# Performance work log

Hardware: AMD Instinct MI355X
Metric: run time of the kernel (lower is better)

Reference implementation:

```python
import jax, jax.numpy as jnp
import numpy as np
from jax import lax

B, HI, WI, D = 8, 64, 64, 128
HO, WO = HI // 2, WI // 2
N_IN, N_OUT = HI * WI, HO * WO
NUM_ITERS = 3
EPS = 1e-6


def _build_indices(Ho, Wo):
    # replicates _build_q_and_in_idx: per coarse position, 9 relative offsets
    dys = np.repeat(np.arange(-1, 2), 3)
    dxs = np.tile(np.arange(-1, 2), 3)
    oy = np.arange(Ho)[:, None, None]
    ox = np.arange(Wo)[None, :, None]
    ny = oy + dys
    nx = ox + dxs
    valid = (ny >= 0) & (ny < Ho) & (nx >= 0) & (nx < Wo)  # (Ho,Wo,9)
    coarse = np.where(valid, ny * Wo + nx, 0)
    base = (oy * Wo + ox) * 9
    g9 = np.where(valid, base + np.arange(9), 0).reshape(-1, 9)
    c9 = coarse.reshape(-1, 9)
    q_idx = np.stack([np.tile(g9, (1, 4))] * 4)
    col_idx = np.stack([np.tile(c9, (1, 4))] * 4)
    in_idx = np.stack([np.tile(np.where(valid, coarse * 4 + h, 0).reshape(-1, 9), (1, 4)) for h in range(4)])
    return q_idx.astype(np.int32), in_idx.astype(np.int32), col_idx.astype(np.int32)


Q_IDX, IN_IDX, COL_IDX = _build_indices(HO, WO)
# NATTEN kernel-3 neighborhoods: window center clamped to stay in-bounds.
NY = np.clip(np.arange(HO) - 1, 0, HO - 3)[:, None] + np.arange(3)  # (HO,3)
NX = np.clip(np.arange(WO) - 1, 0, WO - 3)[:, None] + np.arange(3)  # (WO,3)


def _ln(x, g, b, eps=1e-5):
    mu = x.mean(-1, keepdims=True)
    var = ((x - mu) ** 2).mean(-1, keepdims=True)
    return (x - mu) * lax.rsqrt(var + eps) * g + b


def _forward(x, seed_w, wq, wk, wv, w1, b1, w2, b2, ln_in_g, ln_in_b, ln_out_g, ln_out_b, rpb, tau):
    ny, nx = jnp.asarray(NY), jnp.asarray(NX)
    q_idx = jnp.asarray(Q_IDX)

    def unfold(t):  # (B,HI,WI,D) -> (B,4,HO,WO,D); head = ky*2+kx (F.unfold order)
        return t.reshape(B, HO, 2, WO, 2, D).transpose(0, 2, 4, 1, 3, 5).reshape(B, 4, HO, WO, D)

    k = unfold((_ln(x, ln_in_g, ln_in_b) @ wk.T).reshape(B, HI, WI, D))
    v = unfold((x @ wv.T).reshape(B, HI, WI, D))
    k_n = k[:, :, ny][:, :, :, :, nx]  # (B,4,HO,3,WO,3,D)
    v_n = v[:, :, ny][:, :, :, :, nx]

    x_map = x.reshape(B, HI, WI, D).transpose(0, 3, 1, 2)
    seed = lax.conv_general_dilated(x_map, seed_w, (2, 2), ((1, 1), (1, 1)),
                                    dimension_numbers=('NCHW', 'OIHW', 'NCHW'))
    x_out = _ln(seed.reshape(B, D, N_OUT).transpose(0, 2, 1), ln_out_g, ln_out_b)

    scale = jnp.exp(tau)
    attn36 = a_col_h = None
    for _ in range(NUM_ITERS):
        q = (_ln(x_out, ln_out_g, ln_out_b) @ wq.T).reshape(B, HO, WO, D)
        # na2d_qk (q broadcast over the 4 heads) + relative position bias
        logits = jnp.einsum('byxd,bhykxld->bhyxkl', q, k_n).reshape(B, 4, HO, WO, 9) + rpb.reshape(1, 4, 1, 1, 9)
        attn = jax.nn.softmax(logits * scale, axis=-1) + EPS
        flat = attn.reshape(B, 4, N_OUT * 9)
        attn36 = jnp.take_along_axis(
            flat, jnp.broadcast_to(q_idx.reshape(1, 4, -1), (B, 4, N_OUT * 36)), axis=-1
        ).reshape(B, 4, N_OUT, 36)
        a_col_h = attn36 / (attn36.sum(axis=(1, 3), keepdims=True) + EPS)
        attn9 = a_col_h[..., :9].reshape(B, 4, HO, WO, 3, 3)
        # na2d_av then sum over heads
        updates = jnp.einsum('bhyxkl,bhykxld->byxd', attn9, v_n).reshape(B, N_OUT, D)
        x_out = x_out + updates
        h1 = jax.nn.gelu(x_out @ w1.T + b1, approximate=False)
        x_out = x_out + _ln(h1 @ w2.T + b2, ln_out_g, ln_out_b)
    return x_out, attn36, a_col_h


def setup_inputs() -> dict:
    key = jax.random.key(0)
    ks = jax.random.split(key, 8)
    n = lambda k, shape, s: jax.random.normal(k, shape, jnp.float32) * s
    D2 = 2 * D
    return {
        'x': jax.random.normal(ks[0], (B, N_IN, D), jnp.float32),
        'seed_w': n(ks[1], (D, D, 3, 3), (2.0 / (9 * D)) ** 0.5),
        'wq': n(ks[2], (D, D), D ** -0.5),
        'wk': n(ks[3], (D, D), D ** -0.5),
        'wv': n(ks[4], (D, D), D ** -0.5),
        'w1': n(ks[5], (D2, D), D ** -0.5),
        'b1': jnp.zeros((D2,), jnp.float32),
        'w2': n(ks[6], (D, D2), D2 ** -0.5),
        'b2': jnp.zeros((D,), jnp.float32),
        'ln_in_g': jnp.ones((D,), jnp.float32),
        'ln_in_b': jnp.zeros((D,), jnp.float32),
        'ln_out_g': jnp.ones((D,), jnp.float32),
        'ln_out_b': jnp.zeros((D,), jnp.float32),
        'rpb': n(ks[7], (4, 9), 0.02),
        'tau': jnp.float32(np.log(D ** -0.5)),
    }


def reference(x, seed_w, wq, wk, wv, w1, b1, w2, b2, ln_in_g, ln_in_b, ln_out_g, ln_out_b, rpb, tau):
    x_out, attn36, a_col_h = _forward(x, seed_w, wq, wk, wv, w1, b1, w2, b2,
                                      ln_in_g, ln_in_b, ln_out_g, ln_out_b, rpb, tau)
    # A_col: scatter_add over dim 1 -> A_col[b, in_idx[i,j], j] += a_col_h[b,i,j]
    rows = jnp.asarray(IN_IDX).reshape(4 * N_OUT, 36)
    cols = jnp.broadcast_to(jnp.arange(36), rows.shape)
    A_col = jnp.zeros((B, N_IN, N_OUT), x.dtype).at[:, rows, cols].add(a_col_h.reshape(B, 4 * N_OUT, 36))
    # A_row: scatter_add over dim 2 -> A_row[b, i, col_idx[i,j]] += attn36[b,i,j]
    ri = jnp.broadcast_to(jnp.arange(4 * N_OUT)[:, None], (4 * N_OUT, 36))
    A_row = jnp.zeros((B, N_IN, N_OUT), x.dtype).at[:, ri, jnp.asarray(COL_IDX).reshape(4 * N_OUT, 36)].add(
        attn36.reshape(B, 4 * N_OUT, 36))
    return x_out, A_row, A_col
```

## Files before the change

### kernel.cpp

```cpp
#include <hip/hip_runtime.h>
#include <hip/hip_bf16.h>
#include <math.h>

#define BB   8
#define HI_  64
#define WI_  64
#define DD   128
#define HO_  32
#define WO_  32
#define NIN  4096
#define NOUT 1024
#define LN_EPS 1e-5f
#define ATT_EPS 1e-6f

typedef short bf16x8 __attribute__((ext_vector_type(8)));
typedef float f32x4  __attribute__((ext_vector_type(4)));

__device__ __forceinline__ ushort f2bf(float f) {
    union { float f; unsigned u; } a; a.f = f;
    unsigned u = a.u;
    return (ushort)((u + 0x7FFFu + ((u >> 16) & 1u)) >> 16);
}
__device__ __forceinline__ float bf2f(ushort u) {
    union { unsigned u; float f; } a; a.u = ((unsigned)u) << 16;
    return a.f;
}

__global__ __launch_bounds__(256)
void wconvert_kernel(const float* __restrict__ wq, const float* __restrict__ wk,
                     const float* __restrict__ wv, const float* __restrict__ w1,
                     const float* __restrict__ w2, const float* __restrict__ sw,
                     ushort* __restrict__ dst)
{
    int i = blockIdx.x * 256 + threadIdx.x;
    float v;
    if (i < 16384)        v = wk[i];
    else if (i < 32768)   v = wv[i - 16384];
    else if (i < 49152)   v = wq[i - 32768];
    else if (i < 81920)   v = w1[i - 49152];
    else if (i < 114688)  v = w2[i - 81920];
    else {
        int j = i - 114688;
        int n = j / 1152;
        int rem = j - n * 1152;
        int tap = rem >> 7, di = rem & 127;
        v = sw[((size_t)(n * DD + di)) * 9 + tap];
    }
    dst[i] = f2bf(v);
}

__global__ __launch_bounds__(256)
void prep_kernel(const float* __restrict__ x, const ushort* __restrict__ wkb,
                 const ushort* __restrict__ wvb, const ushort* __restrict__ wcb,
                 const float* __restrict__ ligg, const float* __restrict__ libb,
                 const float* __restrict__ logg, const float* __restrict__ lobb,
                 ushort* __restrict__ kbuf, ushort* __restrict__ vbuf,
                 float* __restrict__ xout)
{
    __shared__ __align__(16) char arena[62208];
    const int tid = threadIdx.x;
    const int wid = tid >> 6, lane = tid & 63;
    const int lr = lane & 15, lk = (lane >> 4) << 3;

    if (blockIdx.x < 512) {
        ushort (*Araw)[136] = (ushort (*)[136])(arena);
        ushort (*Aln)[136]  = (ushort (*)[136])(arena + 17408);
        float  (*rstat)[2]  = (float  (*)[2])(arena + 34816);
        const int row0 = blockIdx.x * 64;

        float4 xv[8];
        #pragma unroll
        for (int i = 0; i < 8; ++i) {
            int l = tid + i * 256;
            int r = l >> 5, c4 = (l & 31) << 2;
            float4 v = *(const float4*)(x + (size_t)(row0 + r) * DD + c4);
            xv[i] = v;
            ushort4 o; o.x = f2bf(v.x); o.y = f2bf(v.y); o.z = f2bf(v.z); o.w = f2bf(v.w);
            *(ushort4*)&Araw[r][c4] = o;
            float s  = v.x + v.y + v.z + v.w;
            float s2 = v.x * v.x + v.y * v.y + v.z * v.z + v.w * v.w;
            #pragma unroll
            for (int o2 = 16; o2 > 0; o2 >>= 1) {
                s  += __shfl_down(s,  o2, 32);
                s2 += __shfl_down(s2, o2, 32);
            }
            if ((tid & 31) == 0) {
                float mu = s * (1.f / DD);
                float var = s2 * (1.f / DD) - mu * mu;
                rstat[r][0] = mu; rstat[r][1] = rsqrtf(var + LN_EPS);
            }
        }
        __syncthreads();
        #pragma unroll
        for (int i = 0; i < 8; ++i) {
            int l = tid + i * 256;
            int r = l >> 5, c4 = (l & 31) << 2;
            float mu = rstat[r][0], rs = rstat[r][1];
            float4 v = xv[i];
            ushort4 o;
            o.x = f2bf((v.x - mu) * rs * ligg[c4 + 0] + libb[c4 + 0]);
            o.y = f2bf((v.y - mu) * rs * ligg[c4 + 1] + libb[c4 + 1]);
            o.z = f2bf((v.z - mu) * rs * ligg[c4 + 2] + libb[c4 + 2]);
            o.w = f2bf((v.w - mu) * rs * ligg[c4 + 3] + libb[c4 + 3]);
            *(ushort4*)&Aln[r][c4] = o;
        }
        __syncthreads();

        const int wm = (wid & 1) * 32, wn = (wid >> 1) * 64;
        f32x4 ak[2][4] = {}, av[2][4] = {};
        #pragma unroll
        for (int ks = 0; ks < 4; ++ks) {
            int kk = ks * 32 + lk;
            bf16x8 aL[2], aR[2];
            #pragma unroll
            for (int mi = 0; mi < 2; ++mi) {
                aL[mi] = *(const bf16x8*)&Aln[wm + mi * 16 + lr][kk];
                aR[mi] = *(const bf16x8*)&Araw[wm + mi * 16 + lr][kk];
            }
            #pragma unroll
            for (int ni = 0; ni < 4; ++ni) {
                bf16x8 bK = *(const bf16x8*)(wkb + (size_t)(wn + ni * 16 + lr) * DD + kk);
                bf16x8 bV = *(const bf16x8*)(wvb + (size_t)(wn + ni * 16 + lr) * DD + kk);
                #pragma unroll
                for (int mi = 0; mi < 2; ++mi) {
                    ak[mi][ni] = __builtin_amdgcn_mfma_f32_16x16x32_bf16(aL[mi], bK, ak[mi][ni], 0, 0, 0);
                    av[mi][ni] = __builtin_amdgcn_mfma_f32_16x16x32_bf16(aR[mi], bV, av[mi][ni], 0, 0, 0);
                }
            }
        }
        #pragma unroll
        for (int mi = 0; mi < 2; ++mi) {
            #pragma unroll
            for (int ni = 0; ni < 4; ++ni) {
                int n = wn + ni * 16 + (lane & 15);
                #pragma unroll
                for (int r = 0; r < 4; ++r) {
                    int m = row0 + wm + mi * 16 + ((lane >> 4) << 2) + r;
                    int b = m >> 12, pix = m & 4095;
                    int iy = pix >> 6, ix = pix & 63;
                    int h = ((iy & 1) << 1) | (ix & 1);
                    int cp = ((iy >> 1) << 5) | (ix >> 1);
                    size_t orow = ((size_t)(b * 4 + h) << 10) + cp;
                    kbuf[orow * DD + n] = f2bf(ak[mi][ni][r]);
                    vbuf[orow * DD + n] = f2bf(av[mi][ni][r]);
                }
            }
        }
    } else {
        ushort (*As)[72]   = (ushort (*)[72])(arena);
        ushort (*Bs)[72]   = (ushort (*)[72])(arena + 9216);
        float  (*es)[132]  = (float  (*)[132])(arena + 27648);
        float  (*rstat)[2] = (float  (*)[2])(arena + 61440);
        const int row0 = (blockIdx.x - 512) * 64;
        const int wm = (wid & 1) * 32, wn = (wid >> 1) * 64;
        f32x4 acc[2][4] = {};

        for (int k0 = 0; k0 < 1152; k0 += 64) {
            #pragma unroll
            for (int i = 0; i < 4; ++i) {
                int l = tid + i * 256;
                int r = l >> 4, c4 = (l & 15) << 2;
                int m = row0 + r;
                int b = m >> 10, p = m & 1023;
                int y = p >> 5, xx = p & 31;
                int kg = k0 + c4;
                int tap = kg >> 7, di = kg & 127;
                int ky = tap / 3, kx = tap - ky * 3;
                int iy = 2 * y + ky - 1, ix = 2 * xx + kx - 1;
                float4 v;
                if ((unsigned)iy < (unsigned)HI_ && (unsigned)ix < (unsigned)WI_)
                    v = *(const float4*)(x + ((size_t)b * NIN + iy * WI_ + ix) * DD + di);
                else v = make_float4(0.f, 0.f, 0.f, 0.f);
                ushort4 o; o.x = f2bf(v.x); o.y = f2bf(v.y); o.z = f2bf(v.z); o.w = f2bf(v.w);
                *(ushort4*)&As[r][c4] = o;
            }
            #pragma unroll
            for (int i = 0; i < 4; ++i) {
                int l = tid + i * 256;
                int r = l >> 3, c8 = (l & 7) << 3;
                *(uint4*)&Bs[r][c8] = *(const uint4*)(wcb + (size_t)r * 1152 + k0 + c8);
            }
            __syncthreads();
            #pragma unroll
            for (int ks = 0; ks < 2; ++ks) {
                int kk = ks * 32 + lk;
                bf16x8 aF[2];
                aF[0] = *(const bf16x8*)&As[wm + lr][kk];
                aF[1] = *(const bf16x8*)&As[wm + 16 + lr][kk];
                #pragma unroll
                for (int ni = 0; ni < 4; ++ni) {
                    bf16x8 bF = *(const bf16x8*)&Bs[wn + ni * 16 + lr][kk];
                    acc[0][ni] = __builtin_amdgcn_mfma_f32_16x16x32_bf16(aF[0], bF, acc[0][ni], 0, 0, 0);
                    acc[1][ni] = __builtin_amdgcn_mfma_f32_16x16x32_bf16(aF[1], bF, acc[1][ni], 0, 0, 0);
                }
            }
            __syncthreads();
        }
        #pragma unroll
        for (int mi = 0; mi < 2; ++mi)
            #pragma unroll
            for (int ni = 0; ni < 4; ++ni) {
                int n = wn + ni * 16 + (lane & 15);
                #pragma unroll
                for (int r = 0; r < 4; ++r)
                    es[wm + mi * 16 + ((lane >> 4) << 2) + r][n] = acc[mi][ni][r];
            }
        __syncthreads();
        {
            int r = tid >> 2, q = tid & 3;
            float s = 0.f, s2 = 0.f;
            #pragma unroll
            for (int c = 0; c < 32; ++c) { float v = es[r][q * 32 + c]; s += v; s2 += v * v; }
            s += __shfl_down(s, 1, 64); s2 += __shfl_down(s2, 1, 64);
            s += __shfl_down(s, 2, 64); s2 += __shfl_down(s2, 2, 64);
            if (q == 0) {
                float mu = s * (1.f / DD);
                float var = s2 * (1.f / DD) - mu * mu;
                rstat[r][0] = mu; rstat[r][1] = rsqrtf(var + LN_EPS);
            }
        }
        __syncthreads();
        #pragma unroll
        for (int i = 0; i < 8; ++i) {
            int l = tid + i * 256;
            int r = l >> 5, c4 = (l & 31) << 2;
            float mu = rstat[r][0], rs = rstat[r][1];
            float4 o;
            o.x = (es[r][c4 + 0] - mu) * rs * logg[c4 + 0] + lobb[c4 + 0];
            o.y = (es[r][c4 + 1] - mu) * rs * logg[c4 + 1] + lobb[c4 + 1];
            o.z = (es[r][c4 + 2] - mu) * rs * logg[c4 + 2] + lobb[c4 + 2];
            o.w = (es[r][c4 + 3] - mu) * rs * logg[c4 + 3] + lobb[c4 + 3];
            *(float4*)(xout + (size_t)(row0 + r) * DD + c4) = o;
        }
    }
}

template<int LAST>
__global__ __launch_bounds__(256)
void iter_kernel(float* __restrict__ xout, const ushort* __restrict__ kbuf,
                 const ushort* __restrict__ vbuf, const ushort* __restrict__ wqb,
                 const ushort* __restrict__ w1b, const ushort* __restrict__ w2b,
                 const float* __restrict__ b1, const float* __restrict__ b2,
                 const float* __restrict__ lg_, const float* __restrict__ lb_,
                 const float* __restrict__ rpb, const float* __restrict__ tau,
                 float* __restrict__ gbuf, float* __restrict__ denb,
                 float* __restrict__ out)
{
    const int bid = blockIdx.x;
    const int b = bid >> 6, cy = (bid >> 1) & 31, cx0 = (bid & 1) << 4;
    const int ry0 = min(max(cy - 1, 0), HO_ - 3);
    const int tid = threadIdx.x;
    const int wid = tid >> 6, lane = tid & 63;
    const int lr = lane & 15, lk = (lane >> 4) << 3;

    __shared__ float  xsf[17][132];
    __shared__ ushort Aq[32][136];
    __shared__ ushort qs[17][136];
    __shared__ float  rstat[17][2];
    __shared__ float  lgp[16][36];
    __shared__ float  lg0[36];
    __shared__ float  sm0[4];
    __shared__ ushort h1s[16][264];
    __shared__ float  es[16][132];

    for (int l = tid; l < 544; l += 256) {
        int r = l >> 5, c4 = (l & 31) << 2;
        int g = b * NOUT + (r < 16 ? cy * 32 + cx0 + r : 0);
        *(float4*)&xsf[r][c4] = *(const float4*)(xout + (size_t)g * DD + c4);
    }
    __syncthreads();
    if (tid < 68) {
        int r = tid >> 2, q = tid & 3;
        float s = 0.f, s2 = 0.f;
        #pragma unroll
        for (int c = 0; c < 32; ++c) { float v = xsf[r][q * 32 + c]; s += v; s2 += v * v; }
        s += __shfl_down(s, 1, 64); s2 += __shfl_down(s2, 1, 64);
        s += __shfl_down(s, 2, 64); s2 += __shfl_down(s2, 2, 64);
        if (q == 0) {
            float mu = s * (1.f / DD);
            float var = s2 * (1.f / DD) - mu * mu;
            rstat[r][0] = mu; rstat[r][1] = rsqrtf(var + LN_EPS);
        }
    }
    __syncthreads();
    for (int l = tid; l < 544; l += 256) {
        int r = l >> 5, c4 = (l & 31) << 2;
        float mu = rstat[r][0], rs = rstat[r][1];
        ushort4 o;
        o.x = f2bf((xsf[r][c4 + 0] - mu) * rs * lg_[c4 + 0] + lb_[c4 + 0]);
        o.y = f2bf((xsf[r][c4 + 1] - mu) * rs * lg_[c4 + 1] + lb_[c4 + 1]);
        o.z = f2bf((xsf[r][c4 + 2] - mu) * rs * lg_[c4 + 2] + lb_[c4 + 2]);
        o.w = f2bf((xsf[r][c4 + 3] - mu) * rs * lg_[c4 + 3] + lb_[c4 + 3]);
        *(ushort4*)&Aq[r][c4] = o;
    }
    __syncthreads();

    {
        const int wn = wid * 32;
        f32x4 acc[2][2] = {};
        #pragma unroll
        for (int ks = 0; ks < 4; ++ks) {
            int kk = ks * 32 + lk;
            bf16x8 aF0 = *(const bf16x8*)&Aq[lr][kk];
            bf16x8 aF1 = *(const bf16x8*)&Aq[16 + lr][kk];
            #pragma unroll
            for (int ni = 0; ni < 2; ++ni) {
                bf16x8 bF = *(const bf16x8*)(wqb + (size_t)(wn + ni * 16 + lr) * DD + kk);
                acc[0][ni] = __builtin_amdgcn_mfma_f32_16x16x32_bf16(aF0, bF, acc[0][ni], 0, 0, 0);
                acc[1][ni] = __builtin_amdgcn_mfma_f32_16x16x32_bf16(aF1, bF, acc[1][ni], 0, 0, 0);
            }
        }
        #pragma unroll
        for (int mi = 0; mi < 2; ++mi)
            #pragma unroll
            for (int ni = 0; ni < 2; ++ni) {
                int n = wn + ni * 16 + (lane & 15);
                #pragma unroll
                for (int r = 0; r < 4; ++r) {
                    int m = mi * 16 + ((lane >> 4) << 2) + r;
                    if (m < 17) qs[m][n] = f2bf(acc[mi][ni][r]);
                }
            }
    }
    __syncthreads();

    for (int task = tid; task < 612; task += 256) {
        const ushort *kp, *qp;
        int cl = 0, h, jj;
        if (task < 576) {
            cl = task / 36; int t2 = task - cl * 36;
            h = t2 / 9; jj = t2 - h * 9;
            int ky = jj / 3, kx = jj - ky * 3;
            int c = cx0 + cl;
            int nx = min(max(c - 1, 0), WO_ - 3) + kx;
            kp = kbuf + (((size_t)(b * 4 + h) << 10) + (ry0 + ky) * 32 + nx) * DD;
            qp = &qs[cl][0];
        } else {
            int t2 = task - 576;
            h = t2 / 9; jj = t2 - h * 9;
            int ky = jj / 3, kx = jj - ky * 3;
            kp = kbuf + (((size_t)(b * 4 + h) << 10) + ky * 32 + kx) * DD;
            qp = &qs[16][0];
        }
        float s = 0.f;
        #pragma unroll 4
        for (int d = 0; d < 128; d += 8) {
            uint4 ku = *(const uint4*)(kp + d);
            uint4 qu = *(const uint4*)(qp + d);
            const ushort* kk2 = (const ushort*)&ku;
            const ushort* qq2 = (const ushort*)&qu;
            #pragma unroll
            for (int t = 0; t < 8; ++t) s += bf2f(kk2[t]) * bf2f(qq2[t]);
        }
        if (task < 576) lgp[cl][h * 9 + jj] = s;
        else            lg0[task - 576] = s;
    }
    __syncthreads();

    if (tid < 68) {
        float scale = expf(tau[0]);
        int h; const float* lptr; int cl = 0;
        if (tid < 64) { cl = tid >> 2; h = tid & 3; lptr = &lgp[cl][h * 9]; }
        else          { h = tid - 64; lptr = &lg0[h * 9]; }
        float tmpv[9], mx = -1e30f;
        #pragma unroll
        for (int jj = 0; jj < 9; ++jj) {
            float v = (lptr[jj] + rpb[h * 9 + jj]) * scale;
            tmpv[jj] = v; mx = fmaxf(mx, v);
        }
        float ss = 0.f;
        #pragma unroll
        for (int jj = 0; jj < 9; ++jj) { tmpv[jj] = expf(tmpv[jj] - mx); ss += tmpv[jj]; }
        float inv = 1.f / ss;
        if (tid < 64) {
            #pragma unroll
            for (int jj = 0; jj < 9; ++jj) lgp[cl][h * 9 + jj] = tmpv[jj] * inv + ATT_EPS;
        } else sm0[h] = tmpv[0] * inv + ATT_EPS;
    }
    __syncthreads();

    if (tid < 64) {
        int cl = tid >> 2, h = tid & 3;
        int c = cx0 + cl;
        float s = 0.f, gv[9];
        #pragma unroll
        for (int jj = 0; jj < 9; ++jj) {
            int dy = jj / 3 - 1, dx = jj % 3 - 1;
            bool valid = ((unsigned)(cy + dy) < (unsigned)HO_) && ((unsigned)(c + dx) < (unsigned)WO_);
            float v = valid ? lgp[cl][h * 9 + jj] : sm0[h];
            gv[jj] = v; s += v;
        }
        float tot = s;
        tot += __shfl_xor(tot, 1, 4);
        tot += __shfl_xor(tot, 2, 4);
        float dd = 4.f * tot + ATT_EPS;
        if (h == 0) denb[b * NOUT + cy * 32 + cx0 + cl] = dd;
        float inv = 1.f / dd;
        float* gp = gbuf + (((size_t)(b * 4 + h) << 10) + cy * 32 + c) * 9;
        #pragma unroll
        for (int jj = 0; jj < 9; ++jj) {
            gp[jj] = gv[jj];
            lgp[cl][h * 9 + jj] = gv[jj] * inv;
        }
    }
    __syncthreads();

    {
        int cl = tid >> 4, d0 = (tid & 15) << 3;
        int c = cx0 + cl;
        int rx0 = min(max(c - 1, 0), WO_ - 3);
        float acc8[8] = {};
        #pragma unroll
        for (int h = 0; h < 4; ++h)
            #pragma unroll
            for (int jj = 0; jj < 9; ++jj) {
                float cf = lgp[cl][h * 9 + jj];
                int ky = jj / 3, kx = jj - ky * 3;
                const ushort* vp = vbuf + (((size_t)(b * 4 + h) << 10) + (ry0 + ky) * 32 + rx0 + kx) * DD + d0;
                uint4 v0 = *(const uint4*)(vp);
                const ushort* vs0 = (const ushort*)&v0;
                #pragma unroll
                for (int t = 0; t < 8; ++t) acc8[t] += cf * bf2f(vs0[t]);
            }
        #pragma unroll
        for (int t = 0; t < 8; t += 4) {
            float4 o = *(float4*)&xsf[cl][d0 + t];
            o.x += acc8[t]; o.y += acc8[t + 1]; o.z += acc8[t + 2]; o.w += acc8[t + 3];
            *(float4*)&xsf[cl][d0 + t] = o;
        }
    }
    __syncthreads();

    for (int l = tid; l < 512; l += 256) {
        int r = l >> 5, c4 = (l & 31) << 2;
        ushort4 o;
        o.x = f2bf(xsf[r][c4 + 0]); o.y = f2bf(xsf[r][c4 + 1]);
        o.z = f2bf(xsf[r][c4 + 2]); o.w = f2bf(xsf[r][c4 + 3]);
        *(ushort4*)&Aq[r][c4] = o;
    }
    __syncthreads();
    {
        const int wn = wid * 64;
        f32x4 acc[4] = {};
        #pragma unroll
        for (int ks = 0; ks < 4; ++ks) {
            int kk = ks * 32 + lk;
            bf16x8 a0 = *(const bf16x8*)&Aq[lr][kk];
            #pragma unroll
            for (int ni = 0; ni < 4; ++ni) {
                bf16x8 bF = *(const bf16x8*)(w1b + (size_t)(wn + ni * 16 + lr) * DD + kk);
                acc[ni] = __builtin_amdgcn_mfma_f32_16x16x32_bf16(a0, bF, acc[ni], 0, 0, 0);
            }
        }
        #pragma unroll
        for (int ni = 0; ni < 4; ++ni) {
            int n = wn + ni * 16 + (lane & 15);
            float bv = b1[n];
            #pragma unroll
            for (int r = 0; r < 4; ++r) {
                int m = ((lane >> 4) << 2) + r;
                float v = acc[ni][r] + bv;
                v = 0.5f * v * (1.f + erff(v * 0.70710678118654752f));
                h1s[m][n] = f2bf(v);
            }
        }
    }
    __syncthreads();

    {
        const int wn = wid * 32;
        f32x4 acc[2] = {};
        #pragma unroll
        for (int ks = 0; ks < 8; ++ks) {
            int kk = ks * 32 + lk;
            bf16x8 a0 = *(const bf16x8*)&h1s[lr][kk];
            #pragma unroll
            for (int ni = 0; ni < 2; ++ni) {
                bf16x8 bF = *(const bf16x8*)(w2b + (size_t)(wn + ni * 16 + lr) * 256 + kk);
                acc[ni] = __builtin_amdgcn_mfma_f32_16x16x32_bf16(a0, bF, acc[ni], 0, 0, 0);
            }
        }
        #pragma unroll
        for (int ni = 0; ni < 2; ++ni) {
            int n = wn + ni * 16 + (lane & 15);
            float bv = b2[n];
            #pragma unroll
            for (int r = 0; r < 4; ++r)
                es[((lane >> 4) << 2) + r][n] = acc[ni][r] + bv;
        }
    }
    __syncthreads();
    if (tid < 128) {
        int r = tid >> 3, qq = tid & 7;
        float s = 0.f, s2 = 0.f;
        #pragma unroll
        for (int c = 0; c < 16; ++c) { float v = es[r][qq * 16 + c]; s += v; s2 += v * v; }
        s += __shfl_down(s, 1, 64); s2 += __shfl_down(s2, 1, 64);
        s += __shfl_down(s, 2, 64); s2 += __shfl_down(s2, 2, 64);
        s += __shfl_down(s, 4, 64); s2 += __shfl_down(s2, 4, 64);
        if (qq == 0) {
            float mu = s * (1.f / DD);
            float var = s2 * (1.f / DD) - mu * mu;
            rstat[r][0] = mu; rstat[r][1] = rsqrtf(var + LN_EPS);
        }
    }
    __syncthreads();
    for (int l = tid; l < 512; l += 256) {
        int r = l >> 5, c4 = (l & 31) << 2;
        float mu = rstat[r][0], rs = rstat[r][1];
        size_t off = ((size_t)(b * NOUT + cy * 32 + cx0 + r)) * DD + c4;
        float4 o;
        o.x = xsf[r][c4 + 0] + (es[r][c4 + 0] - mu) * rs * lg_[c4 + 0] + lb_[c4 + 0];
        o.y = xsf[r][c4 + 1] + (es[r][c4 + 1] - mu) * rs * lg_[c4 + 1] + lb_[c4 + 1];
        o.z = xsf[r][c4 + 2] + (es[r][c4 + 2] - mu) * rs * lg_[c4 + 2] + lb_[c4 + 2];
        o.w = xsf[r][c4 + 3] + (es[r][c4 + 3] - mu) * rs * lg_[c4 + 3] + lb_[c4 + 3];
        *(float4*)(xout + off) = o;
        if (LAST) *(float4*)(out + off) = o;
    }
}

__global__ __launch_bounds__(256)
void arowcol_kernel(const float* __restrict__ gbuf, const float* __restrict__ denb,
                    float* __restrict__ Arow, float* __restrict__ Acol)
{
    const int tid = threadIdx.x;
    __shared__ int   cols[9];
    __shared__ float vals[9];
    __shared__ float wred[9][4];
    if (blockIdx.x < 32768) {
        const int bi = blockIdx.x;
        const int b = bi >> 12, i = bi & 4095;
        const int h = i >> 10, p = i & 1023;
        const int cy = p >> 5, cx = p & 31;
        if (tid < 9) {
            int dy = tid / 3 - 1, dx = tid % 3 - 1;
            bool valid = ((unsigned)(cy + dy) < (unsigned)HO_) && ((unsigned)(cx + dx) < (unsigned)WO_);
            cols[tid] = valid ? (cy + dy) * WO_ + (cx + dx) : 0;
            vals[tid] = 4.f * gbuf[(((size_t)(b * 4 + h) << 10) + p) * 9 + tid];
        }
        __syncthreads();
        float* row = Arow + (size_t)bi * NOUT;
        int c4 = tid << 2;
        float o[4] = {};
        #pragma unroll
        for (int e = 0; e < 4; ++e)
            #pragma unroll
            for (int jj = 0; jj < 9; ++jj)
                if (cols[jj] == c4 + e) o[e] += vals[jj];
        *(float4*)(row + c4) = make_float4(o[0], o[1], o[2], o[3]);
    } else {
        const int br = blockIdx.x - 32768;
        const int b = br >> 12, r = br & 4095;
        const int h = r & 3, coarse = r >> 2;
        const int cy = coarse >> 5, cx = coarse & 31;
        if (tid < 9) {
            int dy = tid / 3 - 1, dx = tid % 3 - 1;
            int py = cy - dy, px = cx - dx;
            float v = 0.f;
            if ((unsigned)py < (unsigned)HO_ && (unsigned)px < (unsigned)WO_) {
                int p = py * WO_ + px;
                v = gbuf[(((size_t)(b * 4 + h) << 10) + p) * 9 + tid] / denb[b * NOUT + p];
            }
            vals[tid] = v;
        }
        if (r == 0) {
            float part[9] = {};
            for (int p = tid; p < NOUT; p += 256) {
                float invd = 1.f / denb[b * NOUT + p];
                int py = p >> 5, px = p & 31;
                #pragma unroll
                for (int jj = 0; jj < 9; ++jj) {
                    int dy = jj / 3 - 1, dx = jj % 3 - 1;
                    bool valid = ((unsigned)(py + dy) < (unsigned)HO_) && ((unsigned)(px + dx) < (unsigned)WO_);
                    if (!valid) part[jj] += invd;
                }
            }
            #pragma unroll
            for (int jj = 0; jj < 9; ++jj) {
                float s = part[jj];
                #pragma unroll
                for (int o = 32; o > 0; o >>= 1) s += __shfl_down(s, o, 64);
                if ((tid & 63) == 0) wred[jj][tid >> 6] = s;
            }
            __syncthreads();
            if (tid < 9) {
                float s = wred[tid][0] + wred[tid][1] + wred[tid][2] + wred[tid][3];
                float H = 0.f;
                for (int h2 = 0; h2 < 4; ++h2)
                    H += gbuf[(((size_t)(b * 4 + h2)) << 10) * 9];
                vals[tid] += H * s;
            }
        }
        __syncthreads();
        float* row = Acol + (size_t)br * NOUT;
        int c4 = tid << 2;
        float o[4];
        #pragma unroll
        for (int e = 0; e < 4; ++e) {
            int c = c4 + e;
            o[e] = (c < 36) ? vals[c % 9] : 0.f;
        }
        *(float4*)(row + c4) = make_float4(o[0], o[1], o[2], o[3]);
    }
}

extern "C" void kernel_launch(void* const* d_in, const int* in_sizes, int n_in,
                              void* d_out, int out_size, void* d_ws, size_t ws_size,
                              hipStream_t stream)
{
    const float* x        = (const float*)d_in[0];
    const float* seed_w   = (const float*)d_in[1];
    const float* wq       = (const float*)d_in[2];
    const float* wk       = (const float*)d_in[3];
    const float* wv       = (const float*)d_in[4];
    const float* w1       = (const float*)d_in[5];
    const float* b1       = (const float*)d_in[6];
    const float* w2       = (const float*)d_in[7];
    const float* b2       = (const float*)d_in[8];
    const float* ln_in_g  = (const float*)d_in[9];
    const float* ln_in_b  = (const float*)d_in[10];
    const float* ln_out_g = (const float*)d_in[11];
    const float* ln_out_b = (const float*)d_in[12];
    const float* rpb      = (const float*)d_in[13];
    const float* tau      = (const float*)d_in[14];

    float* out  = (float*)d_out;
    float* Arow = out + (size_t)BB * NOUT * DD;
    float* Acol = Arow + (size_t)BB * NIN * NOUT;

    float* ws    = (float*)d_ws;
    float* xout  = ws;
    float* gbuf  = xout + (size_t)BB * NOUT * DD;
    float* denb  = gbuf + (size_t)BB * 4 * NOUT * 9;
    ushort* wb   = (ushort*)(denb + BB * NOUT);
    ushort* wkb  = wb;
    ushort* wvb  = wb + 16384;
    ushort* wqb  = wb + 32768;
    ushort* w1b  = wb + 49152;
    ushort* w2b  = wb + 81920;
    ushort* wcb  = wb + 114688;

    ushort* kbuf = (ushort*)Arow;
    ushort* vbuf = kbuf + (size_t)4194304;

    wconvert_kernel<<<1024, 256, 0, stream>>>(wq, wk, wv, w1, w2, seed_w, wb);
    prep_kernel<<<640, 256, 0, stream>>>(x, wkb, wvb, wcb, ln_in_g, ln_in_b,
                                         ln_out_g, ln_out_b, kbuf, vbuf, xout);

    for (int it = 0; it < 3; ++it) {
        if (it < 2)
            iter_kernel<0><<<BB * HO_ * 2, 256, 0, stream>>>(
                xout, kbuf, vbuf, wqb, w1b, w2b, b1, b2, ln_out_g, ln_out_b,
                rpb, tau, gbuf, denb, out);
        else
            iter_kernel<1><<<BB * HO_ * 2, 256, 0, stream>>>(
                xout, kbuf, vbuf, wqb, w1b, w2b, b1, b2, ln_out_g, ln_out_b,
                rpb, tau, gbuf, denb, out);
    }

    arowcol_kernel<<<2 * BB * NIN, 256, 0, stream>>>(gbuf, denb, Arow, Acol);
}
```

Measured before the change: 192.7 us.

## Fold query projection into keys once in prep instead of per iteration

Uses the identity (ln(x) Wq^T)·k = ln(x)·(Wq^T k), precomputing K2 = K·Wq once in the prep kernel with a transposed bf16 Wq. Each of the three iteration kernels then skips its per-block Q projection GEMM and uses the normalized slot features directly as the query. This trades three small GEMMs per iteration for one larger extra GEMM in prep, plus an extra bf16 rounding step on the keys that may shift numerics.

```diff
diff --git a/kernel.cpp b/kernel.cpp
--- a/kernel.cpp
+++ b/kernel.cpp
@@ -36,7 +36,8 @@
     float v;
     if (i < 16384)        v = wk[i];
     else if (i < 32768)   v = wv[i - 16384];
-    else if (i < 49152)   v = wq[i - 32768];
+    else if (i < 49152) { int j = i - 32768; int d = j >> 7, n = j & 127;
+                          v = wq[n * DD + d]; }
     else if (i < 81920)   v = w1[i - 49152];
     else if (i < 114688)  v = w2[i - 81920];
     else {
@@ -51,10 +52,11 @@
 
 __global__ __launch_bounds__(256)
 void prep_kernel(const float* __restrict__ x, const ushort* __restrict__ wkb,
-                 const ushort* __restrict__ wvb, const ushort* __restrict__ wcb,
+                 const ushort* __restrict__ wvb, const ushort* __restrict__ wqTb,
+                 const ushort* __restrict__ wcb,
                  const float* __restrict__ ligg, const float* __restrict__ libb,
                  const float* __restrict__ logg, const float* __restrict__ lobb,
-                 ushort* __restrict__ kbuf, ushort* __restrict__ vbuf,
+                 ushort* __restrict__ k2buf, ushort* __restrict__ vbuf,
                  float* __restrict__ xout)
 {
     __shared__ __align__(16) char arena[62208];
@@ -107,44 +109,90 @@
         __syncthreads();
 
         const int wm = (wid & 1) * 32, wn = (wid >> 1) * 64;
-        f32x4 ak[2][4] = {}, av[2][4] = {};
-        #pragma unroll
-        for (int ks = 0; ks < 4; ++ks) {
-            int kk = ks * 32 + lk;
-            bf16x8 aL[2], aR[2];
-            #pragma unroll
-            for (int mi = 0; mi < 2; ++mi) {
-                aL[mi] = *(const bf16x8*)&Aln[wm + mi * 16 + lr][kk];
-                aR[mi] = *(const bf16x8*)&Araw[wm + mi * 16 + lr][kk];
-            }
-            #pragma unroll
-            for (int ni = 0; ni < 4; ++ni) {
-                bf16x8 bK = *(const bf16x8*)(wkb + (size_t)(wn + ni * 16 + lr) * DD + kk);
-                bf16x8 bV = *(const bf16x8*)(wvb + (size_t)(wn + ni * 16 + lr) * DD + kk);
+        {
+            f32x4 ak[2][4] = {}, av[2][4] = {};
+            #pragma unroll
+            for (int ks = 0; ks < 4; ++ks) {
+                int kk = ks * 32 + lk;
+                bf16x8 aL[2], aR[2];
                 #pragma unroll
                 for (int mi = 0; mi < 2; ++mi) {
-                    ak[mi][ni] = __builtin_amdgcn_mfma_f32_16x16x32_bf16(aL[mi], bK, ak[mi][ni], 0, 0, 0);
-                    av[mi][ni] = __builtin_amdgcn_mfma_f32_16x16x32_bf16(aR[mi], bV, av[mi][ni], 0, 0, 0);
-                }
-            }
-        }
-        #pragma unroll
-        for (int mi = 0; mi < 2; ++mi) {
-            #pragma unroll
-            for (int ni = 0; ni < 4; ++ni) {
-                int n = wn + ni * 16 + (lane & 15);
-                #pragma unroll
-                for (int r = 0; r < 4; ++r) {
-                    int m = row0 + wm + mi * 16 + ((lane >> 4) << 2) + r;
-                    int b = m >> 12, pix = m & 4095;
-                    int iy = pix >> 6, ix = pix & 63;
-                    int h = ((iy & 1) << 1) | (ix & 1);
-                    int cp = ((iy >> 1) << 5) | (ix >> 1);
-                    size_t orow = ((size_t)(b * 4 + h) << 10) + cp;
-                    kbuf[orow * DD + n] = f2bf(ak[mi][ni][r]);
-                    vbuf[orow * DD + n] = f2bf(av[mi][ni][r]);
-                }
-            }
+                    aL[mi] = *(const bf16x8*)&Aln[wm + mi * 16 + lr][kk];
+                    aR[mi] = *(const bf16x8*)&Araw[wm + mi * 16 + lr][kk];
+                }
+                #pragma unroll
+                for (int ni = 0; ni < 4; ++ni) {
+                    bf16x8 bK = *(const bf16x8*)(wkb + (size_t)(wn + ni * 16 + lr) * DD + kk);
+                    bf16x8 bV = *(const bf16x8*)(wvb + (size_t)(wn + ni * 16 + lr) * DD + kk);
+                    #pragma unroll
+                    for (int mi = 0; mi < 2; ++mi) {
+                        ak[mi][ni] = __builtin_amdgcn_mfma_f32_16x16x32_bf16(aL[mi], bK, ak[mi][ni], 0, 0, 0);
+                        av[mi][ni] = __builtin_amdgcn_mfma_f32_16x16x32_bf16(aR[mi], bV, av[mi][ni], 0, 0, 0);
+                    }
+                }
+            }
+            #pragma unroll
+            for (int mi = 0; mi < 2; ++mi)
+                #pragma unroll
+                for (int ni = 0; ni < 4; ++ni) {
+                    int n = wn + ni * 16 + (lane & 15);
+                    #pragma unroll
+                    for (int r = 0; r < 4; ++r) {
+                        int m = row0 + wm + mi * 16 + ((lane >> 4) << 2) + r;
+                        int b = m >> 12, pix = m & 4095;
+                        int iy = pix >> 6, ix = pix & 63;
+                        int h = ((iy & 1) << 1) | (ix & 1);
+                        int cp = ((iy >> 1) << 5) | (ix >> 1);
+                        size_t orow = ((size_t)(b * 4 + h) << 10) + cp;
+                        vbuf[orow * DD + n] = f2bf(av[mi][ni][r]);
+                    }
+                }
+            __syncthreads();
+            #pragma unroll
+            for (int mi = 0; mi < 2; ++mi)
+                #pragma unroll
+                for (int ni = 0; ni < 4; ++ni) {
+                    int n = wn + ni * 16 + (lane & 15);
+                    #pragma unroll
+                    for (int r = 0; r < 4; ++r) {
+                        int lm = wm + mi * 16 + ((lane >> 4) << 2) + r;
+                        Aln[lm][n] = f2bf(ak[mi][ni][r]);
+                    }
+                }
+        }
+        __syncthreads();
+
+        {
+            f32x4 a2[2][4] = {};
+            #pragma unroll
+            for (int ks = 0; ks < 4; ++ks) {
+                int kk = ks * 32 + lk;
+                bf16x8 aF[2];
+                aF[0] = *(const bf16x8*)&Aln[wm + lr][kk];
+                aF[1] = *(const bf16x8*)&Aln[wm + 16 + lr][kk];
+                #pragma unroll
+                for (int ni = 0; ni < 4; ++ni) {
+                    bf16x8 bF = *(const bf16x8*)(wqTb + (size_t)(wn + ni * 16 + lr) * DD + kk);
+                    a2[0][ni] = __builtin_amdgcn_mfma_f32_16x16x32_bf16(aF[0], bF, a2[0][ni], 0, 0, 0);
+                    a2[1][ni] = __builtin_amdgcn_mfma_f32_16x16x32_bf16(aF[1], bF, a2[1][ni], 0, 0, 0);
+                }
+            }
+            #pragma unroll
+            for (int mi = 0; mi < 2; ++mi)
+                #pragma unroll
+                for (int ni = 0; ni < 4; ++ni) {
+                    int n = wn + ni * 16 + (lane & 15);
+                    #pragma unroll
+                    for (int r = 0; r < 4; ++r) {
+                        int m = row0 + wm + mi * 16 + ((lane >> 4) << 2) + r;
+                        int b = m >> 12, pix = m & 4095;
+                        int iy = pix >> 6, ix = pix & 63;
+                        int h = ((iy & 1) << 1) | (ix & 1);
+                        int cp = ((iy >> 1) << 5) | (ix >> 1);
+                        size_t orow = ((size_t)(b * 4 + h) << 10) + cp;
+                        k2buf[orow * DD + n] = f2bf(a2[mi][ni][r]);
+                    }
+                }
         }
     } else {
         ushort (*As)[72]   = (ushort (*)[72])(arena);
@@ -237,8 +285,8 @@
 
 template<int LAST>
 __global__ __launch_bounds__(256)
-void iter_kernel(float* __restrict__ xout, const ushort* __restrict__ kbuf,
-                 const ushort* __restrict__ vbuf, const ushort* __restrict__ wqb,
+void iter_kernel(float* __restrict__ xout, const ushort* __restrict__ k2buf,
+                 const ushort* __restrict__ vbuf,
                  const ushort* __restrict__ w1b, const ushort* __restrict__ w2b,
                  const float* __restrict__ b1, const float* __restrict__ b2,
                  const float* __restrict__ lg_, const float* __restrict__ lb_,
@@ -254,7 +302,6 @@
     const int lr = lane & 15, lk = (lane >> 4) << 3;
 
     __shared__ float  xsf[17][132];
-    __shared__ ushort Aq[32][136];
     __shared__ ushort qs[17][136];
     __shared__ float  rstat[17][2];
     __shared__ float  lgp[16][36];
@@ -291,36 +338,7 @@
         o.y = f2bf((xsf[r][c4 + 1] - mu) * rs * lg_[c4 + 1] + lb_[c4 + 1]);
         o.z = f2bf((xsf[r][c4 + 2] - mu) * rs * lg_[c4 + 2] + lb_[c4 + 2]);
         o.w = f2bf((xsf[r][c4 + 3] - mu) * rs * lg_[c4 + 3] + lb_[c4 + 3]);
-        *(ushort4*)&Aq[r][c4] = o;
-    }
-    __syncthreads();
-
-    {
-        const int wn = wid * 32;
-        f32x4 acc[2][2] = {};
-        #pragma unroll
-        for (int ks = 0; ks < 4; ++ks) {
-            int kk = ks * 32 + lk;
-            bf16x8 aF0 = *(const bf16x8*)&Aq[lr][kk];
-            bf16x8 aF1 = *(const bf16x8*)&Aq[16 + lr][kk];
-            #pragma unroll
-            for (int ni = 0; ni < 2; ++ni) {
-                bf16x8 bF = *(const bf16x8*)(wqb + (size_t)(wn + ni * 16 + lr) * DD + kk);
-                acc[0][ni] = __builtin_amdgcn_mfma_f32_16x16x32_bf16(aF0, bF, acc[0][ni], 0, 0, 0);
-                acc[1][ni] = __builtin_amdgcn_mfma_f32_16x16x32_bf16(aF1, bF, acc[1][ni], 0, 0, 0);
-            }
-        }
-        #pragma unroll
-        for (int mi = 0; mi < 2; ++mi)
-            #pragma unroll
-            for (int ni = 0; ni < 2; ++ni) {
-                int n = wn + ni * 16 + (lane & 15);
-                #pragma unroll
-                for (int r = 0; r < 4; ++r) {
-                    int m = mi * 16 + ((lane >> 4) << 2) + r;
-                    if (m < 17) qs[m][n] = f2bf(acc[mi][ni][r]);
-                }
-            }
+        *(ushort4*)&qs[r][c4] = o;
     }
     __syncthreads();
 
@@ -333,13 +351,13 @@
             int ky = jj / 3, kx = jj - ky * 3;
             int c = cx0 + cl;
             int nx = min(max(c - 1, 0), WO_ - 3) + kx;
-            kp = kbuf + (((size_t)(b * 4 + h) << 10) + (ry0 + ky) * 32 + nx) * DD;
+            kp = k2buf + (((size_t)(b * 4 + h) << 10) + (ry0 + ky) * 32 + nx) * DD;
             qp = &qs[cl][0];
         } else {
             int t2 = task - 576;
             h = t2 / 9; jj = t2 - h * 9;
             int ky = jj / 3, kx = jj - ky * 3;
-            kp = kbuf + (((size_t)(b * 4 + h) << 10) + ky * 32 + kx) * DD;
+            kp = k2buf + (((size_t)(b * 4 + h) << 10) + ky * 32 + kx) * DD;
             qp = &qs[16][0];
         }
         float s = 0.f;
@@ -436,7 +454,7 @@
         ushort4 o;
         o.x = f2bf(xsf[r][c4 + 0]); o.y = f2bf(xsf[r][c4 + 1]);
         o.z = f2bf(xsf[r][c4 + 2]); o.w = f2bf(xsf[r][c4 + 3]);
-        *(ushort4*)&Aq[r][c4] = o;
+        *(ushort4*)&qs[r][c4] = o;
     }
     __syncthreads();
     {
@@ -445,7 +463,7 @@
         #pragma unroll
         for (int ks = 0; ks < 4; ++ks) {
             int kk = ks * 32 + lk;
-            bf16x8 a0 = *(const bf16x8*)&Aq[lr][kk];
+            bf16x8 a0 = *(const bf16x8*)&qs[lr][kk];
             #pragma unroll
             for (int ni = 0; ni < 4; ++ni) {
                 bf16x8 bF = *(const bf16x8*)(w1b + (size_t)(wn + ni * 16 + lr) * DD + kk);
@@ -635,26 +653,26 @@
     ushort* wb   = (ushort*)(denb + BB * NOUT);
     ushort* wkb  = wb;
     ushort* wvb  = wb + 16384;
-    ushort* wqb  = wb + 32768;
+    ushort* wqTb = wb + 32768;
     ushort* w1b  = wb + 49152;
     ushort* w2b  = wb + 81920;
     ushort* wcb  = wb + 114688;
 
-    ushort* kbuf = (ushort*)Arow;
-    ushort* vbuf = kbuf + (size_t)4194304;
+    ushort* k2buf = (ushort*)Arow;
+    ushort* vbuf  = k2buf + (size_t)4194304;
 
     wconvert_kernel<<<1024, 256, 0, stream>>>(wq, wk, wv, w1, w2, seed_w, wb);
-    prep_kernel<<<640, 256, 0, stream>>>(x, wkb, wvb, wcb, ln_in_g, ln_in_b,
-                                         ln_out_g, ln_out_b, kbuf, vbuf, xout);
+    prep_kernel<<<640, 256, 0, stream>>>(x, wkb, wvb, wqTb, wcb, ln_in_g, ln_in_b,
+                                         ln_out_g, ln_out_b, k2buf, vbuf, xout);
 
     for (int it = 0; it < 3; ++it) {
         if (it < 2)
             iter_kernel<0><<<BB * HO_ * 2, 256, 0, stream>>>(
-                xout, kbuf, vbuf, wqb, w1b, w2b, b1, b2, ln_out_g, ln_out_b,
+                xout, k2buf, vbuf, w1b, w2b, b1, b2, ln_out_g, ln_out_b,
                 rpb, tau, gbuf, denb, out);
         else
             iter_kernel<1><<<BB * HO_ * 2, 256, 0, stream>>>(
-                xout, kbuf, vbuf, wqb, w1b, w2b, b1, b2, ln_out_g, ln_out_b,
+                xout, k2buf, vbuf, w1b, w2b, b1, b2, ln_out_g, ln_out_b,
                 rpb, tau, gbuf, denb, out);
     }
 
```

New measurement: 191.9 us. No clear change (-0.4%).
